# Kernel tuning notes

Measured on AMD Instinct MI355X. Metric: run time of the kernel, lower is better.

Reference implementation:

```python
import jax, jax.numpy as jnp
import numpy as np


def setup_inputs() -> dict:
    key = jax.random.key(0)
    k = jax.random.split(key, 5)
    bs, n_heads, ch, n_obj, emb = 4, 8, 64, 8, 64
    ih = iw = 32
    T = ih * iw
    return {
        "qkv": jax.random.normal(k[0], (bs, 3 * n_heads * ch, T), dtype=jnp.float32),
        "bboxes": jax.random.uniform(k[1], (bs, n_obj, 5), dtype=jnp.float32),
        "null_prompt_emb": jax.random.normal(k[2], (bs, emb, T), dtype=jnp.float32),
        "prompt_emb": jax.random.normal(k[3], (bs, emb, T), dtype=jnp.float32),
        "W_prompt": jax.random.normal(k[4], (3 * n_heads * ch, emb), dtype=jnp.float32) * 0.02,
        "n_heads": n_heads,
        "image_h": ih,
        "image_w": iw,
    }


def _region_masks(bboxes, h, w):
    # Faithful translation of get_region: bbox unpacked as (x, y, width, height, obj_idx).
    # Returns float masks [b, n_obj, h*w].
    x, y, bw, bh = bboxes[..., 0], bboxes[..., 1], bboxes[..., 2], bboxes[..., 3]
    i0 = jnp.minimum(float(h) - 1.0, jnp.floor(y * h))
    j0 = jnp.minimum(float(w) - 1.0, jnp.floor(x * w))
    i1 = i0 + jnp.maximum(1.0, jnp.ceil(bh * h))
    j1 = j0 + jnp.maximum(1.0, jnp.ceil(bw * w))
    ii = jnp.arange(h, dtype=jnp.float32)
    jj = jnp.arange(w, dtype=jnp.float32)
    mi = (ii >= i0[..., None]) & (ii < i1[..., None])          # [b, n, h]
    mj = (jj >= j0[..., None]) & (jj < j1[..., None])          # [b, n, w]
    m = (mi[..., :, None] & mj[..., None, :]).astype(jnp.float32)  # [b, n, h, w]
    return m.reshape(m.shape[0], m.shape[1], h * w)


def reference(qkv, bboxes, null_prompt_emb, prompt_emb, W_prompt, n_heads, image_h, image_w):
    bs, width, T = qkv.shape
    ch = width // (3 * n_heads)
    scale = float(ch) ** -0.25  # 1/sqrt(sqrt(ch))

    def split3(x):
        x = x.reshape(bs * n_heads, 3 * ch, T)
        return x[:, :ch], x[:, ch:2 * ch], x[:, 2 * ch:]

    q, k, v = split3(qkv)
    # to_prompt_token is a 1x1 Conv1d (no bias) == matmul over the channel dim
    nq, nk, nv = split3(jnp.einsum('oc,bct->bot', W_prompt, null_prompt_emb))
    pq, pk, pv = split3(jnp.einsum('oc,bct->bot', W_prompt, prompt_emb))

    def attn(qh, kh, vh, col_mask=None):
        w = jnp.einsum('bct,bcs->bts', qh * scale, kh * scale)
        if col_mask is not None:
            w = jnp.where(col_mask[:, None, :] > 0.5, w, -1e9)
        w = jax.nn.softmax(w.astype(jnp.float32), axis=-1).astype(qh.dtype)
        return jnp.einsum('bts,bcs->btc', w, vh)  # [bs*heads, T, ch]

    # global (null-prompt) attention
    a_null = attn(q + nq, k + nk, v + nv)

    # per-object masked attention, blended by region masks
    masks = _region_masks(bboxes, image_h, image_w)       # [bs, n_obj, T]
    masks = jnp.repeat(masks, n_heads, axis=0)            # [(bs*heads), n_obj, T]
    qf, kf, vf = q + pq, k + pk, v + pv
    a_fg = jnp.zeros_like(a_null)
    counter = jnp.zeros((bs * n_heads, T, 1), dtype=jnp.float32)
    for o in range(masks.shape[1]):  # small fixed loop over objects
        m = masks[:, o]                                   # [bs*heads, T]
        a_fg = a_fg + m[:, :, None] * attn(qf, kf, vf, col_mask=m)
        counter = counter + m[:, :, None]
    fg = counter > 0.5
    a_final = jnp.where(fg, a_fg, a_null) / jnp.where(fg, counter, 1.0)
    return jnp.transpose(a_final, (0, 2, 1)).reshape(bs, n_heads * ch, T)
```

## Files before the change

kernel.cpp:

```cpp
#include <hip/hip_runtime.h>

#define BS 4
#define NH 8
#define TT 1024
#define WROWS 1536
#define NOBJ 8
#define NT 65536

#define QNT_OFF  0
#define KNT_OFF  2097152
#define VNCS_OFF 4194304
#define QFT_OFF  6291456
#define KFT_OFF  8388608
#define VFT_OFF  10485760

typedef __attribute__((ext_vector_type(8))) short short8;
typedef __attribute__((ext_vector_type(4))) float v4f;

__device__ __forceinline__ short f2bf(float f) {
    unsigned u = __float_as_uint(f);
    u = (u + 0x7FFF + ((u >> 16) & 1)) >> 16;
    return (short)u;
}
__device__ __forceinline__ unsigned cvtpk(float a, float b) {
    unsigned u;
    asm("v_cvt_pk_bf16_f32 %0, %1, %2" : "=v"(u) : "v"(a), "v"(b));
    return u;
}
__device__ __forceinline__ float fexp2(float x) {
    float r;
    asm("v_exp_f32 %0, %1" : "=v"(r) : "v"(x));
    return r;
}
__device__ __forceinline__ int pi64(int s) { return 4 * (s & 15) + (s >> 4); }

__device__ __forceinline__ void get_region(const float* __restrict__ bb,
                                           int& i0, int& j0, int& hh, int& ww) {
    float x = bb[0], y = bb[1], bw = bb[2], bh = bb[3];
    float i0f = fminf(31.0f, floorf(y * 32.0f));
    float j0f = fminf(31.0f, floorf(x * 32.0f));
    float i1f = i0f + fmaxf(1.0f, ceilf(bh * 32.0f));
    float j1f = j0f + fmaxf(1.0f, ceilf(bw * 32.0f));
    i0 = (int)i0f; j0 = (int)j0f;
    int i1 = min(32, (int)i1f);
    int j1 = min(32, (int)j1f);
    hh = i1 - i0; ww = j1 - j0;
}

__global__ __launch_bounds__(256)
void fuse_kernel(const float* __restrict__ qkv, const float* __restrict__ nEmb,
                 const float* __restrict__ pEmb, const float* __restrict__ W,
                 short* __restrict__ wsS) {
    __shared__ __align__(16) short Ent[64 * 72];
    __shared__ __align__(16) short Ept[64 * 72];
    __shared__ __align__(16) short sbuf[64 * 72];
    int t0 = blockIdx.x * 64;
    int r0 = blockIdx.y * 64;
    int b  = blockIdx.z;
    int tid = threadIdx.x;
    int w = tid >> 6, lane = tid & 63, ln = lane & 15, qd = lane >> 4;

    {
        int e  = tid >> 4;
        int t4 = (tid & 15) * 4;
#pragma unroll
        for (int p = 0; p < 4; ++p) {
            int ee = p * 16 + e;
            float4 n4 = *(const float4*)&nEmb[(b * 64 + ee) * TT + t0 + t4];
            float4 p4 = *(const float4*)&pEmb[(b * 64 + ee) * TT + t0 + t4];
            Ent[(t4 + 0) * 72 + ee] = f2bf(n4.x); Ent[(t4 + 1) * 72 + ee] = f2bf(n4.y);
            Ent[(t4 + 2) * 72 + ee] = f2bf(n4.z); Ent[(t4 + 3) * 72 + ee] = f2bf(n4.w);
            Ept[(t4 + 0) * 72 + ee] = f2bf(p4.x); Ept[(t4 + 1) * 72 + ee] = f2bf(p4.y);
            Ept[(t4 + 2) * 72 + ee] = f2bf(p4.z); Ept[(t4 + 3) * 72 + ee] = f2bf(p4.w);
        }
    }
    short8 aw0, aw1;
    {
        const float* wp = &W[(r0 + 16 * w + ln) * 64 + qd * 8];
        float4 f0 = *(const float4*)wp;
        float4 f1 = *(const float4*)(wp + 4);
        float4 f2 = *(const float4*)(wp + 32);
        float4 f3 = *(const float4*)(wp + 36);
        uint4 u0, u1;
        u0.x = cvtpk(f0.x, f0.y); u0.y = cvtpk(f0.z, f0.w);
        u0.z = cvtpk(f1.x, f1.y); u0.w = cvtpk(f1.z, f1.w);
        u1.x = cvtpk(f2.x, f2.y); u1.y = cvtpk(f2.z, f2.w);
        u1.z = cvtpk(f3.x, f3.y); u1.w = cvtpk(f3.z, f3.w);
        aw0 = *(short8*)&u0; aw1 = *(short8*)&u1;
    }
    __syncthreads();
    v4f accN[4], accP[4];
#pragma unroll
    for (int nn = 0; nn < 4; ++nn) {
        const short* bp = &Ent[(nn * 16 + ln) * 72 + qd * 8];
        short8 b0 = *(const short8*)bp;
        short8 b1 = *(const short8*)(bp + 32);
        v4f z = (v4f){0.f, 0.f, 0.f, 0.f};
        z = __builtin_amdgcn_mfma_f32_16x16x32_bf16(aw0, b0, z, 0, 0, 0);
        z = __builtin_amdgcn_mfma_f32_16x16x32_bf16(aw1, b1, z, 0, 0, 0);
        accN[nn] = z;
        const short* cp = &Ept[(nn * 16 + ln) * 72 + qd * 8];
        short8 c0 = *(const short8*)cp;
        short8 c1 = *(const short8*)(cp + 32);
        v4f y = (v4f){0.f, 0.f, 0.f, 0.f};
        y = __builtin_amdgcn_mfma_f32_16x16x32_bf16(aw0, c0, y, 0, 0, 0);
        y = __builtin_amdgcn_mfma_f32_16x16x32_bf16(aw1, c1, y, 0, 0, 0);
        accP[nn] = y;
    }
    int sec = (r0 % 192) / 64;
    int h = r0 / 192, bh = b * 8 + h;
    float sc = (sec == 0) ? 0.18033688f : 1.0f;
    float xan[4][4], xap[4][4];
#pragma unroll
    for (int nn = 0; nn < 4; ++nn)
#pragma unroll
        for (int i = 0; i < 4; ++i) {
            int r = r0 + 16 * w + 4 * qd + i;
            float x = qkv[(b * WROWS + r) * TT + t0 + nn * 16 + ln];
            xan[nn][i] = (accN[nn][i] + x) * sc;
            xap[nn][i] = (accP[nn][i] + x) * sc;
        }

    if (sec == 2) {
        short* Vn = wsS + VNCS_OFF + bh * NT;
        __syncthreads();
#pragma unroll
        for (int nn = 0; nn < 4; ++nn)
#pragma unroll
            for (int i = 0; i < 4; ++i)
                sbuf[(16 * w + 4 * qd + i) * 72 + 4 * ln + nn] = f2bf(xan[nn][i]);
        __syncthreads();
#pragma unroll
        for (int rep = 0; rep < 2; ++rep) {
            int idx = rep * 256 + tid; int cl = idx >> 3, c8 = idx & 7;
            *(short8*)&Vn[cl * TT + t0 + c8 * 8] = *(const short8*)&sbuf[cl * 72 + c8 * 8];
        }
        __syncthreads();
        short* dst = wsS + VFT_OFF + bh * NT + t0 * 64;
#pragma unroll
        for (int nn = 0; nn < 4; ++nn) {
            uint2 u; u.x = cvtpk(xap[nn][0], xap[nn][1]); u.y = cvtpk(xap[nn][2], xap[nn][3]);
            *(uint2*)&sbuf[(nn * 16 + ln) * 72 + 16 * w + 4 * qd] = u;
        }
        __syncthreads();
#pragma unroll
        for (int rep = 0; rep < 2; ++rep) {
            int idx = rep * 256 + tid; int tl = idx >> 3, c8 = idx & 7;
            *(short8*)&dst[tl * 64 + c8 * 8] = *(const short8*)&sbuf[tl * 72 + c8 * 8];
        }
    } else {
        short* dn = wsS + (sec == 0 ? QNT_OFF : KNT_OFF) + bh * NT + t0 * 64;
        short* df = wsS + (sec == 0 ? QFT_OFF : KFT_OFF) + bh * NT + t0 * 64;
        __syncthreads();
#pragma unroll
        for (int nn = 0; nn < 4; ++nn) {
            uint2 u; u.x = cvtpk(xan[nn][0], xan[nn][1]); u.y = cvtpk(xan[nn][2], xan[nn][3]);
            *(uint2*)&sbuf[(nn * 16 + ln) * 72 + 16 * w + 4 * qd] = u;
        }
        __syncthreads();
#pragma unroll
        for (int rep = 0; rep < 2; ++rep) {
            int idx = rep * 256 + tid; int tl = idx >> 3, c8 = idx & 7;
            *(short8*)&dn[tl * 64 + c8 * 8] = *(const short8*)&sbuf[tl * 72 + c8 * 8];
        }
        __syncthreads();
#pragma unroll
        for (int nn = 0; nn < 4; ++nn) {
            uint2 u; u.x = cvtpk(xap[nn][0], xap[nn][1]); u.y = cvtpk(xap[nn][2], xap[nn][3]);
            *(uint2*)&sbuf[(nn * 16 + ln) * 72 + 16 * w + 4 * qd] = u;
        }
        __syncthreads();
#pragma unroll
        for (int rep = 0; rep < 2; ++rep) {
            int idx = rep * 256 + tid; int tl = idx >> 3, c8 = idx & 7;
            *(short8*)&df[tl * 64 + c8 * 8] = *(const short8*)&sbuf[tl * 72 + c8 * 8];
        }
    }
}

__global__ __launch_bounds__(256)
void attn_fused(const short* __restrict__ wsS, const float* __restrict__ bboxes,
                float* __restrict__ out) {
    __shared__ __align__(16) short lds[13824];
    __shared__ unsigned short tmap[1024];
    short* Qs = lds;
    short* Ks = lds + 4608;
    short* Vs = lds + 9216;
    int bh = blockIdx.x, rt = blockIdx.y;
    int b = bh >> 3, h = bh & 7;
    int t0 = rt * 64;
    int tid = threadIdx.x;
    int w = tid >> 6, lane = tid & 63, ln = lane & 15, qd = lane >> 4;
    const short* QnT = wsS + QNT_OFF + bh * NT;
    const short* KnT = wsS + KNT_OFF + bh * NT;
    const short* Vn  = wsS + VNCS_OFF + bh * NT;
    const short* QfT = wsS + QFT_OFF + bh * NT;
    const short* KfT = wsS + KFT_OFF + bh * NT;
    const short* VfT = wsS + VFT_OFF + bh * NT;
    int sidx = tid, scell = sidx >> 3, sc8 = sidx & 7;
    int sidx2 = 256 + tid, scell2 = sidx2 >> 3, sc82 = sidx2 & 7;

    *(short8*)&Qs[scell * 72 + sc8 * 8]  = *(const short8*)&QnT[(t0 + scell) * 64 + sc8 * 8];
    *(short8*)&Qs[scell2 * 72 + sc82 * 8] = *(const short8*)&QnT[(t0 + scell2) * 64 + sc82 * 8];
    __syncthreads();
    short8 aq0 = *(const short8*)&Qs[(16 * w + ln) * 72 + qd * 8];
    short8 aq1 = *(const short8*)&Qs[(16 * w + ln) * 72 + 32 + qd * 8];
    v4f O[4]; float l[4];
#pragma unroll
    for (int r = 0; r < 4; ++r) l[r] = 0.f;
#pragma unroll
    for (int cc = 0; cc < 4; ++cc) O[cc] = (v4f){0.f, 0.f, 0.f, 0.f};
    short8 kreg[2], vreg[2];
    kreg[0] = *(const short8*)&KnT[scell * 64 + sc8 * 8];
    kreg[1] = *(const short8*)&KnT[scell2 * 64 + sc82 * 8];
    vreg[0] = *(const short8*)&Vn[scell * TT + sc8 * 8];
    vreg[1] = *(const short8*)&Vn[scell2 * TT + sc82 * 8];
    for (int ct = 0; ct < 16; ++ct) {
        __syncthreads();
        *(short8*)&Ks[scell * 72 + sc8 * 8]  = kreg[0];
        *(short8*)&Ks[scell2 * 72 + sc82 * 8] = kreg[1];
        *(short8*)&Vs[scell * 72 + sc8 * 8]  = vreg[0];
        *(short8*)&Vs[scell2 * 72 + sc82 * 8] = vreg[1];
        __syncthreads();
        if (ct < 15) {
            int s0 = (ct + 1) * 64;
            kreg[0] = *(const short8*)&KnT[(s0 + scell) * 64 + sc8 * 8];
            kreg[1] = *(const short8*)&KnT[(s0 + scell2) * 64 + sc82 * 8];
            vreg[0] = *(const short8*)&Vn[scell * TT + s0 + sc8 * 8];
            vreg[1] = *(const short8*)&Vn[scell2 * TT + s0 + sc82 * 8];
        }
        v4f S[4];
#pragma unroll
        for (int nn = 0; nn < 4; ++nn) {
            short8 b0 = *(const short8*)&Ks[(nn * 16 + ln) * 72 + qd * 8];
            short8 b1 = *(const short8*)&Ks[(nn * 16 + ln) * 72 + 32 + qd * 8];
            v4f z = (v4f){0.f, 0.f, 0.f, 0.f};
            z = __builtin_amdgcn_mfma_f32_16x16x32_bf16(aq0, b0, z, 0, 0, 0);
            z = __builtin_amdgcn_mfma_f32_16x16x32_bf16(aq1, b1, z, 0, 0, 0);
            S[nn] = z;
        }
#pragma unroll
        for (int r = 0; r < 4; ++r) {
            float e0 = fexp2(S[0][r]);
            float e1 = fexp2(S[1][r]);
            float e2 = fexp2(S[2][r]);
            float e3 = fexp2(S[3][r]);
            l[r] += (e0 + e1) + (e2 + e3);
            uint2 u; u.x = cvtpk(e0, e1); u.y = cvtpk(e2, e3);
            *(uint2*)&Qs[(w * 16 + 4 * qd + r) * 72 + 4 * ln] = u;
        }
        short8 ap0 = *(const short8*)&Qs[(w * 16 + ln) * 72 + qd * 8];
        short8 ap1 = *(const short8*)&Qs[(w * 16 + ln) * 72 + 32 + qd * 8];
#pragma unroll
        for (int cc = 0; cc < 4; ++cc) {
            short8 bv0 = *(const short8*)&Vs[(cc * 16 + ln) * 72 + qd * 8];
            short8 bv1 = *(const short8*)&Vs[(cc * 16 + ln) * 72 + 32 + qd * 8];
            O[cc] = __builtin_amdgcn_mfma_f32_16x16x32_bf16(ap0, bv0, O[cc], 0, 0, 0);
            O[cc] = __builtin_amdgcn_mfma_f32_16x16x32_bf16(ap1, bv1, O[cc], 0, 0, 0);
        }
    }
    v4f Onull[4];
#pragma unroll
    for (int r = 0; r < 4; ++r) {
        float rs = l[r];
        rs += __shfl_xor(rs, 1, 64);
        rs += __shfl_xor(rs, 2, 64);
        rs += __shfl_xor(rs, 4, 64);
        rs += __shfl_xor(rs, 8, 64);
        float inv = 1.0f / rs;
#pragma unroll
        for (int cc = 0; cc < 4; ++cc) Onull[cc][r] = O[cc][r] * inv;
    }

    __syncthreads();
    *(short8*)&Qs[scell * 72 + sc8 * 8]  = *(const short8*)&QfT[(t0 + scell) * 64 + sc8 * 8];
    *(short8*)&Qs[scell2 * 72 + sc82 * 8] = *(const short8*)&QfT[(t0 + scell2) * 64 + sc82 * 8];
    __syncthreads();
    aq0 = *(const short8*)&Qs[(16 * w + ln) * 72 + qd * 8];
    aq1 = *(const short8*)&Qs[(16 * w + ln) * 72 + 32 + qd * 8];
    v4f Oacc[4]; float cnt[4];
#pragma unroll
    for (int r = 0; r < 4; ++r) cnt[r] = 0.f;
#pragma unroll
    for (int cc = 0; cc < 4; ++cc) Oacc[cc] = (v4f){0.f, 0.f, 0.f, 0.f};

    for (int o = 0; o < NOBJ; ++o) {
        int i0, j0, hh, ww;
        get_region(&bboxes[(b * NOBJ + o) * 5], i0, j0, hh, ww);
        int i1 = i0 + hh;
        if (i0 > 2 * rt + 1 || i1 <= 2 * rt) continue;
        int R = hh * ww;
        for (int idx = tid; idx < R; idx += 256) {
            int ri = idx / ww; int rj = idx - ri * ww;
            tmap[idx] = (unsigned short)((i0 + ri) * 32 + j0 + rj);
        }
        __syncthreads();
#pragma unroll
        for (int r = 0; r < 4; ++r) l[r] = 0.f;
#pragma unroll
        for (int cc = 0; cc < 4; ++cc) O[cc] = (v4f){0.f, 0.f, 0.f, 0.f};
        int nct = (R + 63) >> 6;
        {
            int tA = tmap[min(scell, R - 1)];
            int tB = tmap[min(scell2, R - 1)];
            kreg[0] = *(const short8*)&KfT[tA * 64 + sc8 * 8];
            kreg[1] = *(const short8*)&KfT[tB * 64 + sc82 * 8];
            vreg[0] = *(const short8*)&VfT[tA * 64 + sc8 * 8];
            vreg[1] = *(const short8*)&VfT[tB * 64 + sc82 * 8];
        }
        int pA = pi64(scell), pB = pi64(scell2);
        for (int ct = 0; ct < nct; ++ct) {
            int sb = ct * 64;
            __syncthreads();
            *(short8*)&Ks[scell * 72 + sc8 * 8]  = kreg[0];
            *(short8*)&Ks[scell2 * 72 + sc82 * 8] = kreg[1];
#pragma unroll
            for (int jj = 0; jj < 8; ++jj) {
                int j = (jj + sc8) & 7;
                Vs[(sc8 * 8 + j) * 72 + pA] = vreg[0][j];
            }
#pragma unroll
            for (int jj = 0; jj < 8; ++jj) {
                int j = (jj + sc82) & 7;
                Vs[(sc82 * 8 + j) * 72 + pB] = vreg[1][j];
            }
            __syncthreads();
            if (ct + 1 < nct) {
                int s0 = sb + 64;
                int tA = tmap[min(s0 + scell, R - 1)];
                int tB = tmap[min(s0 + scell2, R - 1)];
                kreg[0] = *(const short8*)&KfT[tA * 64 + sc8 * 8];
                kreg[1] = *(const short8*)&KfT[tB * 64 + sc82 * 8];
                vreg[0] = *(const short8*)&VfT[tA * 64 + sc8 * 8];
                vreg[1] = *(const short8*)&VfT[tB * 64 + sc82 * 8];
            }
            v4f S[4];
#pragma unroll
            for (int nn = 0; nn < 4; ++nn) {
                short8 b0 = *(const short8*)&Ks[(nn * 16 + ln) * 72 + qd * 8];
                short8 b1 = *(const short8*)&Ks[(nn * 16 + ln) * 72 + 32 + qd * 8];
                v4f z = (v4f){0.f, 0.f, 0.f, 0.f};
                z = __builtin_amdgcn_mfma_f32_16x16x32_bf16(aq0, b0, z, 0, 0, 0);
                z = __builtin_amdgcn_mfma_f32_16x16x32_bf16(aq1, b1, z, 0, 0, 0);
                S[nn] = z;
            }
            float v0 = (sb +  0 + ln) < R ? 1.f : 0.f;
            float v1 = (sb + 16 + ln) < R ? 1.f : 0.f;
            float v2 = (sb + 32 + ln) < R ? 1.f : 0.f;
            float v3 = (sb + 48 + ln) < R ? 1.f : 0.f;
#pragma unroll
            for (int r = 0; r < 4; ++r) {
                float e0 = fexp2(S[0][r]) * v0;
                float e1 = fexp2(S[1][r]) * v1;
                float e2 = fexp2(S[2][r]) * v2;
                float e3 = fexp2(S[3][r]) * v3;
                l[r] += (e0 + e1) + (e2 + e3);
                uint2 u; u.x = cvtpk(e0, e1); u.y = cvtpk(e2, e3);
                *(uint2*)&Qs[(w * 16 + 4 * qd + r) * 72 + 4 * ln] = u;
            }
            short8 ap0 = *(const short8*)&Qs[(w * 16 + ln) * 72 + qd * 8];
            short8 ap1 = *(const short8*)&Qs[(w * 16 + ln) * 72 + 32 + qd * 8];
#pragma unroll
            for (int cc = 0; cc < 4; ++cc) {
                short8 bv0 = *(const short8*)&Vs[(cc * 16 + ln) * 72 + qd * 8];
                short8 bv1 = *(const short8*)&Vs[(cc * 16 + ln) * 72 + 32 + qd * 8];
                O[cc] = __builtin_amdgcn_mfma_f32_16x16x32_bf16(ap0, bv0, O[cc], 0, 0, 0);
                O[cc] = __builtin_amdgcn_mfma_f32_16x16x32_bf16(ap1, bv1, O[cc], 0, 0, 0);
            }
        }
#pragma unroll
        for (int r = 0; r < 4; ++r) {
            float rs = l[r];
            rs += __shfl_xor(rs, 1, 64);
            rs += __shfl_xor(rs, 2, 64);
            rs += __shfl_xor(rs, 4, 64);
            rs += __shfl_xor(rs, 8, 64);
            float inv = 1.0f / rs;
            int t = t0 + 16 * w + 4 * qd + r;
            int ti = t >> 5, tj = t & 31;
            bool in = (ti >= i0) && (ti < i1) && (tj >= j0) && (tj < j0 + ww);
            if (in) {
                cnt[r] += 1.f;
#pragma unroll
                for (int cc = 0; cc < 4; ++cc) Oacc[cc][r] += O[cc][r] * inv;
            }
        }
    }

    __syncthreads();
    float* Ot = (float*)lds;
#pragma unroll
    for (int r = 0; r < 4; ++r) {
        int tl = 16 * w + 4 * qd + r;
        float icnt = cnt[r] > 0.f ? 1.0f / cnt[r] : 0.f;
#pragma unroll
        for (int cc = 0; cc < 4; ++cc) {
            float val = cnt[r] > 0.f ? Oacc[cc][r] * icnt : Onull[cc][r];
            Ot[(cc * 16 + ln) * 68 + tl] = val;
        }
    }
    __syncthreads();
    int obase = (b * 512 + h * 64) * TT + t0;
#pragma unroll
    for (int rep = 0; rep < 4; ++rep) {
        int idx = rep * 256 + tid; int c = idx >> 4, t4 = (idx & 15) * 4;
        *(float4*)&out[obase + c * TT + t4] = *(float4*)&Ot[c * 68 + t4];
    }
}

extern "C" void kernel_launch(void* const* d_in, const int* in_sizes, int n_in,
                              void* d_out, int out_size, void* d_ws, size_t ws_size,
                              hipStream_t stream) {
    const float* qkv    = (const float*)d_in[0];
    const float* bboxes = (const float*)d_in[1];
    const float* nEmb   = (const float*)d_in[2];
    const float* pEmb   = (const float*)d_in[3];
    const float* W      = (const float*)d_in[4];
    short* wsS = (short*)d_ws;
    float* out = (float*)d_out;

    fuse_kernel<<<dim3(16, 24, 4), 256, 0, stream>>>(qkv, nEmb, pEmb, W, wsS);
    attn_fused<<<dim3(32, 16), 256, 0, stream>>>(wsS, bboxes, out);
}
```

Before: 148.3 us.

## Double-buffer K/V tiles in LDS to halve barriers per attention tile

Adds a second LDS buffer for K and V tiles in both the null-prompt and per-object attention loops. The next tile is written into the alternate buffer while the current one is consumed, and register prefetch now runs two tiles ahead. This cuts the loop to one __syncthreads per tile instead of two. In exchange LDS use grows from about 27KB to about 46KB per block, which may lower occupancy.

Result: no change. 148.9 us (+0.4%).

```diff
diff --git a/kernel.cpp b/kernel.cpp
--- a/kernel.cpp
+++ b/kernel.cpp
@@ -181,11 +181,13 @@
 __global__ __launch_bounds__(256)
 void attn_fused(const short* __restrict__ wsS, const float* __restrict__ bboxes,
                 float* __restrict__ out) {
-    __shared__ __align__(16) short lds[13824];
+    __shared__ __align__(16) short lds[23040];
     __shared__ unsigned short tmap[1024];
-    short* Qs = lds;
-    short* Ks = lds + 4608;
-    short* Vs = lds + 9216;
+    short* Qs  = lds;
+    short* Kb0 = lds + 4608;
+    short* Kb1 = lds + 9216;
+    short* Vb0 = lds + 13824;
+    short* Vb1 = lds + 18432;
     int bh = blockIdx.x, rt = blockIdx.y;
     int b = bh >> 3, h = bh & 7;
     int t0 = rt * 64;
@@ -215,15 +217,28 @@
     kreg[1] = *(const short8*)&KnT[scell2 * 64 + sc82 * 8];
     vreg[0] = *(const short8*)&Vn[scell * TT + sc8 * 8];
     vreg[1] = *(const short8*)&Vn[scell2 * TT + sc82 * 8];
+    *(short8*)&Kb0[scell * 72 + sc8 * 8]  = kreg[0];
+    *(short8*)&Kb0[scell2 * 72 + sc82 * 8] = kreg[1];
+    *(short8*)&Vb0[scell * 72 + sc8 * 8]  = vreg[0];
+    *(short8*)&Vb0[scell2 * 72 + sc82 * 8] = vreg[1];
+    kreg[0] = *(const short8*)&KnT[(64 + scell) * 64 + sc8 * 8];
+    kreg[1] = *(const short8*)&KnT[(64 + scell2) * 64 + sc82 * 8];
+    vreg[0] = *(const short8*)&Vn[scell * TT + 64 + sc8 * 8];
+    vreg[1] = *(const short8*)&Vn[scell2 * TT + 64 + sc82 * 8];
+    __syncthreads();
     for (int ct = 0; ct < 16; ++ct) {
-        __syncthreads();
-        *(short8*)&Ks[scell * 72 + sc8 * 8]  = kreg[0];
-        *(short8*)&Ks[scell2 * 72 + sc82 * 8] = kreg[1];
-        *(short8*)&Vs[scell * 72 + sc8 * 8]  = vreg[0];
-        *(short8*)&Vs[scell2 * 72 + sc82 * 8] = vreg[1];
-        __syncthreads();
+        const short* Kc = (ct & 1) ? Kb1 : Kb0;
+        const short* Vc = (ct & 1) ? Vb1 : Vb0;
+        short* Kn_ = (ct & 1) ? Kb0 : Kb1;
+        short* Vn_ = (ct & 1) ? Vb0 : Vb1;
         if (ct < 15) {
-            int s0 = (ct + 1) * 64;
+            *(short8*)&Kn_[scell * 72 + sc8 * 8]  = kreg[0];
+            *(short8*)&Kn_[scell2 * 72 + sc82 * 8] = kreg[1];
+            *(short8*)&Vn_[scell * 72 + sc8 * 8]  = vreg[0];
+            *(short8*)&Vn_[scell2 * 72 + sc82 * 8] = vreg[1];
+        }
+        if (ct < 14) {
+            int s0 = (ct + 2) * 64;
             kreg[0] = *(const short8*)&KnT[(s0 + scell) * 64 + sc8 * 8];
             kreg[1] = *(const short8*)&KnT[(s0 + scell2) * 64 + sc82 * 8];
             vreg[0] = *(const short8*)&Vn[scell * TT + s0 + sc8 * 8];
@@ -232,8 +247,8 @@
         v4f S[4];
 #pragma unroll
         for (int nn = 0; nn < 4; ++nn) {
-            short8 b0 = *(const short8*)&Ks[(nn * 16 + ln) * 72 + qd * 8];
-            short8 b1 = *(const short8*)&Ks[(nn * 16 + ln) * 72 + 32 + qd * 8];
+            short8 b0 = *(const short8*)&Kc[(nn * 16 + ln) * 72 + qd * 8];
+            short8 b1 = *(const short8*)&Kc[(nn * 16 + ln) * 72 + 32 + qd * 8];
             v4f z = (v4f){0.f, 0.f, 0.f, 0.f};
             z = __builtin_amdgcn_mfma_f32_16x16x32_bf16(aq0, b0, z, 0, 0, 0);
             z = __builtin_amdgcn_mfma_f32_16x16x32_bf16(aq1, b1, z, 0, 0, 0);
@@ -253,11 +268,12 @@
         short8 ap1 = *(const short8*)&Qs[(w * 16 + ln) * 72 + 32 + qd * 8];
 #pragma unroll
         for (int cc = 0; cc < 4; ++cc) {
-            short8 bv0 = *(const short8*)&Vs[(cc * 16 + ln) * 72 + qd * 8];
-            short8 bv1 = *(const short8*)&Vs[(cc * 16 + ln) * 72 + 32 + qd * 8];
+            short8 bv0 = *(const short8*)&Vc[(cc * 16 + ln) * 72 + qd * 8];
+            short8 bv1 = *(const short8*)&Vc[(cc * 16 + ln) * 72 + 32 + qd * 8];
             O[cc] = __builtin_amdgcn_mfma_f32_16x16x32_bf16(ap0, bv0, O[cc], 0, 0, 0);
             O[cc] = __builtin_amdgcn_mfma_f32_16x16x32_bf16(ap1, bv1, O[cc], 0, 0, 0);
         }
+        __syncthreads();
     }
     v4f Onull[4];
 #pragma unroll
@@ -272,7 +288,6 @@
         for (int cc = 0; cc < 4; ++cc) Onull[cc][r] = O[cc][r] * inv;
     }
 
-    __syncthreads();
     *(short8*)&Qs[scell * 72 + sc8 * 8]  = *(const short8*)&QfT[(t0 + scell) * 64 + sc8 * 8];
     *(short8*)&Qs[scell2 * 72 + sc82 * 8] = *(const short8*)&QfT[(t0 + scell2) * 64 + sc82 * 8];
     __syncthreads();
@@ -283,6 +298,7 @@
     for (int r = 0; r < 4; ++r) cnt[r] = 0.f;
 #pragma unroll
     for (int cc = 0; cc < 4; ++cc) Oacc[cc] = (v4f){0.f, 0.f, 0.f, 0.f};
+    int pA = pi64(scell), pB = pi64(scell2);
 
     for (int o = 0; o < NOBJ; ++o) {
         int i0, j0, hh, ww;
@@ -308,25 +324,49 @@
             vreg[0] = *(const short8*)&VfT[tA * 64 + sc8 * 8];
             vreg[1] = *(const short8*)&VfT[tB * 64 + sc82 * 8];
         }
-        int pA = pi64(scell), pB = pi64(scell2);
+        *(short8*)&Kb0[scell * 72 + sc8 * 8]  = kreg[0];
+        *(short8*)&Kb0[scell2 * 72 + sc82 * 8] = kreg[1];
+#pragma unroll
+        for (int jj = 0; jj < 8; ++jj) {
+            int j = (jj + sc8) & 7;
+            Vb0[(sc8 * 8 + j) * 72 + pA] = vreg[0][j];
+        }
+#pragma unroll
+        for (int jj = 0; jj < 8; ++jj) {
+            int j = (jj + sc82) & 7;
+            Vb0[(sc82 * 8 + j) * 72 + pB] = vreg[1][j];
+        }
+        if (nct > 1) {
+            int tA = tmap[min(64 + scell, R - 1)];
+            int tB = tmap[min(64 + scell2, R - 1)];
+            kreg[0] = *(const short8*)&KfT[tA * 64 + sc8 * 8];
+            kreg[1] = *(const short8*)&KfT[tB * 64 + sc82 * 8];
+            vreg[0] = *(const short8*)&VfT[tA * 64 + sc8 * 8];
+            vreg[1] = *(const short8*)&VfT[tB * 64 + sc82 * 8];
+        }
+        __syncthreads();
         for (int ct = 0; ct < nct; ++ct) {
             int sb = ct * 64;
-            __syncthreads();
-            *(short8*)&Ks[scell * 72 + sc8 * 8]  = kreg[0];
-            *(short8*)&Ks[scell2 * 72 + sc82 * 8] = kreg[1];
-#pragma unroll
-            for (int jj = 0; jj < 8; ++jj) {
-                int j = (jj + sc8) & 7;
-                Vs[(sc8 * 8 + j) * 72 + pA] = vreg[0][j];
-            }
-#pragma unroll
-            for (int jj = 0; jj < 8; ++jj) {
-                int j = (jj + sc82) & 7;
-                Vs[(sc82 * 8 + j) * 72 + pB] = vreg[1][j];
-            }
-            __syncthreads();
+            const short* Kc = (ct & 1) ? Kb1 : Kb0;
+            const short* Vc = (ct & 1) ? Vb1 : Vb0;
+            short* Kn_ = (ct & 1) ? Kb0 : Kb1;
+            short* Vn_ = (ct & 1) ? Vb0 : Vb1;
             if (ct + 1 < nct) {
-                int s0 = sb + 64;
+                *(short8*)&Kn_[scell * 72 + sc8 * 8]  = kreg[0];
+                *(short8*)&Kn_[scell2 * 72 + sc82 * 8] = kreg[1];
+#pragma unroll
+                for (int jj = 0; jj < 8; ++jj) {
+                    int j = (jj + sc8) & 7;
+                    Vn_[(sc8 * 8 + j) * 72 + pA] = vreg[0][j];
+                }
+#pragma unroll
+                for (int jj = 0; jj < 8; ++jj) {
+                    int j = (jj + sc82) & 7;
+                    Vn_[(sc82 * 8 + j) * 72 + pB] = vreg[1][j];
+                }
+            }
+            if (ct + 2 < nct) {
+                int s0 = sb + 128;
                 int tA = tmap[min(s0 + scell, R - 1)];
                 int tB = tmap[min(s0 + scell2, R - 1)];
                 kreg[0] = *(const short8*)&KfT[tA * 64 + sc8 * 8];
@@ -337,8 +377,8 @@
             v4f S[4];
 #pragma unroll
             for (int nn = 0; nn < 4; ++nn) {
-                short8 b0 = *(const short8*)&Ks[(nn * 16 + ln) * 72 + qd * 8];
-                short8 b1 = *(const short8*)&Ks[(nn * 16 + ln) * 72 + 32 + qd * 8];
+                short8 b0 = *(const short8*)&Kc[(nn * 16 + ln) * 72 + qd * 8];
+                short8 b1 = *(const short8*)&Kc[(nn * 16 + ln) * 72 + 32 + qd * 8];
                 v4f z = (v4f){0.f, 0.f, 0.f, 0.f};
                 z = __builtin_amdgcn_mfma_f32_16x16x32_bf16(aq0, b0, z, 0, 0, 0);
                 z = __builtin_amdgcn_mfma_f32_16x16x32_bf16(aq1, b1, z, 0, 0, 0);
@@ -362,11 +402,12 @@
             short8 ap1 = *(const short8*)&Qs[(w * 16 + ln) * 72 + 32 + qd * 8];
 #pragma unroll
             for (int cc = 0; cc < 4; ++cc) {
-                short8 bv0 = *(const short8*)&Vs[(cc * 16 + ln) * 72 + qd * 8];
-                short8 bv1 = *(const short8*)&Vs[(cc * 16 + ln) * 72 + 32 + qd * 8];
+                short8 bv0 = *(const short8*)&Vc[(cc * 16 + ln) * 72 + qd * 8];
+                short8 bv1 = *(const short8*)&Vc[(cc * 16 + ln) * 72 + 32 + qd * 8];
                 O[cc] = __builtin_amdgcn_mfma_f32_16x16x32_bf16(ap0, bv0, O[cc], 0, 0, 0);
                 O[cc] = __builtin_amdgcn_mfma_f32_16x16x32_bf16(ap1, bv1, O[cc], 0, 0, 0);
             }
+            __syncthreads();
         }
 #pragma unroll
         for (int r = 0; r < 4; ++r) {
```
